# Kernel tuning notes

Hardware: AMD Instinct MI355X
Metric: run time of the kernel (lower is better)

The kernel has to match this reference:

```python
import jax, jax.numpy as jnp
import numpy as np

B, DE, T = 32, 256, 32
H, W, C = 128, 128, 128  # units == C


def setup_inputs() -> dict:
    key = jax.random.key(0)
    k1, k2, k3 = jax.random.split(key, 3)
    e = jax.random.normal(k1, (B, DE, T), dtype=jnp.float32)
    h = jax.random.normal(k2, (B, H, W, C), dtype=jnp.float32)
    Wd = jax.random.normal(k3, (DE, C), dtype=jnp.float32) * (1.0 / np.sqrt(DE))
    b = jnp.zeros((C,), dtype=jnp.float32)
    return {"e": e, "h": h, "Wd": Wd, "b": b}


def reference(e, h, Wd, b):
    # e: [B, DE, T]  -> dense over DE -> e_: [B, C, T]
    e_ = jnp.einsum('bdt,dc->bct', e, Wd) + b[None, :, None]
    Bh, Hh, Wh, Ch = h.shape
    HW = Hh * Wh
    # h NHWC -> [B, C, HW]
    h1 = h.transpose(0, 3, 1, 2).reshape(Bh, Ch, HW)
    # scores: [B, T, HW], contraction over channels
    s = jnp.einsum('bct,bcn->btn', e_, h1)
    # softmax over T (axis=1)
    beta = jax.nn.softmax(s, axis=1)
    # context: [B, C, HW]
    c = jnp.einsum('bct,btn->bcn', e_, beta)
    # -> [B, HW, C] -> NHWC
    c = c.transpose(0, 2, 1).reshape(Bh, Hh, Wh, Ch)
    return jnp.concatenate([c, h], axis=3)  # [B, H, W, 2C]
```

## Files before the change

### kernel.cpp

```cpp
#include <hip/hip_runtime.h>

typedef float v2f __attribute__((ext_vector_type(2)));

#define B_   32
#define DE_  256
#define T_   32
#define C_   128
#define HW_  16384

__device__ inline v2f vfma2(v2f a, v2f b, v2f c) {
#if __has_builtin(__builtin_elementwise_fma)
    return __builtin_elementwise_fma(a, b, c);
#else
    v2f r; r.x = fmaf(a.x, b.x, c.x); r.y = fmaf(a.y, b.y, c.y); return r;
#endif
}

__global__ __launch_bounds__(256) void dense_e_kernel(
    const float* __restrict__ e, const float* __restrict__ Wd,
    const float* __restrict__ bias, float* __restrict__ ews)
{
    __shared__ float elds[DE_ * T_];
    __shared__ float wlds[DE_ * 16];
    const int b   = blockIdx.y;
    const int cq  = blockIdx.x;
    const int tid = threadIdx.x;

    {
        const float4* erow = (const float4*)(e + ((size_t)b * DE_ + tid) * T_);
        float4* edst = (float4*)(elds + tid * T_);
        #pragma unroll
        for (int i = 0; i < 8; ++i) edst[i] = erow[i];

        const float4* wrow = (const float4*)(Wd + (size_t)tid * C_ + cq * 16);
        float4* wdst = (float4*)(wlds + tid * 16);
        #pragma unroll
        for (int i = 0; i < 4; ++i) wdst[i] = wrow[i];
    }
    __syncthreads();

    const int t  = tid & 31;
    const int c8 = tid >> 5;
    float a0 = 0.f, a1 = 0.f;
    #pragma unroll 8
    for (int d = 0; d < DE_; ++d) {
        float ev = elds[d * T_ + t];
        a0 = fmaf(ev, wlds[d * 16 + c8],     a0);
        a1 = fmaf(ev, wlds[d * 16 + 8 + c8], a1);
    }
    const int c0 = cq * 16 + c8;
    a0 += bias[c0];
    a1 += bias[c0 + 8];
    ews[((size_t)b * C_ + c0)     * T_ + t] = a0;
    ews[((size_t)b * C_ + c0 + 8) * T_ + t] = a1;
}

__global__ __launch_bounds__(256) void attn_fused_kernel(
    const float* __restrict__ h,
    const float* __restrict__ ews,
    float* __restrict__ out)
{
    const int b = blockIdx.x >> 6;
    const int n = ((blockIdx.x & 63) << 8) | threadIdx.x;
    const float* __restrict__ eb = ews + (size_t)b * (C_ * T_);
    const float4* hrow = (const float4*)(h + ((size_t)b * HW_ + n) * C_);
    float4* orow = (float4*)(out + ((size_t)b * HW_ + n) * (2 * C_));

    v2f s2[16];
    #pragma unroll
    for (int i = 0; i < 16; ++i) s2[i] = (v2f){0.f, 0.f};

    #pragma unroll 4
    for (int cb = 0; cb < 32; ++cb) {
        float4 hv = hrow[cb];
        orow[32 + cb] = hv;
        float hc[4] = {hv.x, hv.y, hv.z, hv.w};
        #pragma unroll
        for (int q = 0; q < 4; ++q) {
            const v2f* er = (const v2f*)(eb + (cb * 4 + q) * T_);
            v2f hb = {hc[q], hc[q]};
            #pragma unroll
            for (int tp = 0; tp < 16; ++tp) s2[tp] = vfma2(hb, er[tp], s2[tp]);
        }
    }

    v2f m2 = s2[0];
    #pragma unroll
    for (int i = 1; i < 16; ++i) {
        m2.x = fmaxf(m2.x, s2[i].x);
        m2.y = fmaxf(m2.y, s2[i].y);
    }
    const float m = fmaxf(m2.x, m2.y);
    float l = 0.f;
    #pragma unroll
    for (int i = 0; i < 16; ++i) {
        v2f p;
        p.x = __expf(s2[i].x - m);
        p.y = __expf(s2[i].y - m);
        s2[i] = p;
        l += p.x + p.y;
    }
    const float inv = 1.0f / l;
    #pragma unroll
    for (int i = 0; i < 16; ++i) { s2[i].x *= inv; s2[i].y *= inv; }

    #pragma unroll 4
    for (int cb = 0; cb < 32; ++cb) {
        float r[4];
        #pragma unroll
        for (int q = 0; q < 4; ++q) {
            const v2f* er = (const v2f*)(eb + (cb * 4 + q) * T_);
            v2f a = {0.f, 0.f};
            #pragma unroll
            for (int tp = 0; tp < 16; ++tp) a = vfma2(er[tp], s2[tp], a);
            r[q] = a.x + a.y;
        }
        float4 st = {r[0], r[1], r[2], r[3]};
        orow[cb] = st;
    }
}

extern "C" void kernel_launch(void* const* d_in, const int* in_sizes, int n_in,
                              void* d_out, int out_size, void* d_ws, size_t ws_size,
                              hipStream_t stream) {
    const float* e    = (const float*)d_in[0];
    const float* h    = (const float*)d_in[1];
    const float* Wd   = (const float*)d_in[2];
    const float* bias = (const float*)d_in[3];
    float* ews = (float*)d_ws;
    float* out = (float*)d_out;

    dense_e_kernel<<<dim3(8, 32), 256, 0, stream>>>(e, Wd, bias, ews);
    attn_fused_kernel<<<dim3(32 * (HW_ / 256)), 256, 0, stream>>>(h, ews, out);
}
```

Before: 910.4 us.

## Stage h loads and context stores through padded LDS for coalesced global access

The attention kernel previously had each thread read and write its own 512-byte pixel row, so a wavefront's global accesses were strided across rows. It now loads 32-channel slabs of h cooperatively with coalesced float4 reads and transposes them through padded shared memory. The context output goes back the same way before coalesced stores. This costs about 32KB of LDS per block, extra barriers and LDS traffic, which may lower occupancy.

```diff
diff --git a/kernel.cpp b/kernel.cpp
--- a/kernel.cpp
+++ b/kernel.cpp
@@ -7,6 +7,8 @@
 #define T_   32
 #define C_   128
 #define HW_  16384
+
+#define LSTRIDE 257
 
 __device__ inline v2f vfma2(v2f a, v2f b, v2f c) {
 #if __has_builtin(__builtin_elementwise_fma)
@@ -60,28 +62,48 @@
     const float* __restrict__ ews,
     float* __restrict__ out)
 {
-    const int b = blockIdx.x >> 6;
-    const int n = ((blockIdx.x & 63) << 8) | threadIdx.x;
+    __shared__ float lds[32 * LSTRIDE];
+    const int b   = blockIdx.x >> 6;
+    const int n0  = (blockIdx.x & 63) << 8;
+    const int tid = threadIdx.x;
     const float* __restrict__ eb = ews + (size_t)b * (C_ * T_);
-    const float4* hrow = (const float4*)(h + ((size_t)b * HW_ + n) * C_);
-    float4* orow = (float4*)(out + ((size_t)b * HW_ + n) * (2 * C_));
+    const float* __restrict__ hb = h   + ((size_t)b * HW_ + n0) * C_;
+    float* __restrict__       ob = out + ((size_t)b * HW_ + n0) * (2 * C_);
 
     v2f s2[16];
     #pragma unroll
     for (int i = 0; i < 16; ++i) s2[i] = (v2f){0.f, 0.f};
 
-    #pragma unroll 4
-    for (int cb = 0; cb < 32; ++cb) {
-        float4 hv = hrow[cb];
-        orow[32 + cb] = hv;
-        float hc[4] = {hv.x, hv.y, hv.z, hv.w};
+    for (int cb = 0; cb < 4; ++cb) {
+        float4 hv[8];
         #pragma unroll
-        for (int q = 0; q < 4; ++q) {
-            const v2f* er = (const v2f*)(eb + (cb * 4 + q) * T_);
-            v2f hb = {hc[q], hc[q]};
+        for (int i = 0; i < 8; ++i) {
+            const int idx = i * 256 + tid;
+            hv[i] = *(const float4*)(hb + (size_t)(idx >> 3) * C_ + cb * 32 + (idx & 7) * 4);
+        }
+        #pragma unroll
+        for (int i = 0; i < 8; ++i) {
+            const int idx = i * 256 + tid;
+            const int row = idx >> 3, c4 = idx & 7;
+            *(float4*)(ob + (size_t)row * (2 * C_) + C_ + cb * 32 + c4 * 4) = hv[i];
+            float* dst = lds + (c4 * 4) * LSTRIDE + row;
+            dst[0]           = hv[i].x;
+            dst[LSTRIDE]     = hv[i].y;
+            dst[2 * LSTRIDE] = hv[i].z;
+            dst[3 * LSTRIDE] = hv[i].w;
+        }
+        __syncthreads();
+
+        const float* ec = eb + (cb * 32) * T_;
+        #pragma unroll
+        for (int c = 0; c < 32; ++c) {
+            const float hc = lds[c * LSTRIDE + tid];
+            const v2f* er = (const v2f*)(ec + c * T_);
+            const v2f hbv = {hc, hc};
             #pragma unroll
-            for (int tp = 0; tp < 16; ++tp) s2[tp] = vfma2(hb, er[tp], s2[tp]);
+            for (int tp = 0; tp < 16; ++tp) s2[tp] = vfma2(hbv, er[tp], s2[tp]);
         }
+        __syncthreads();
     }
 
     v2f m2 = s2[0];
@@ -104,19 +126,25 @@
     #pragma unroll
     for (int i = 0; i < 16; ++i) { s2[i].x *= inv; s2[i].y *= inv; }
 
-    #pragma unroll 4
-    for (int cb = 0; cb < 32; ++cb) {
-        float r[4];
+    for (int cb = 0; cb < 4; ++cb) {
         #pragma unroll
-        for (int q = 0; q < 4; ++q) {
-            const v2f* er = (const v2f*)(eb + (cb * 4 + q) * T_);
+        for (int c = 0; c < 32; ++c) {
+            const v2f* er = (const v2f*)(eb + (size_t)(cb * 32 + c) * T_);
             v2f a = {0.f, 0.f};
             #pragma unroll
             for (int tp = 0; tp < 16; ++tp) a = vfma2(er[tp], s2[tp], a);
-            r[q] = a.x + a.y;
+            lds[c * LSTRIDE + tid] = a.x + a.y;
         }
-        float4 st = {r[0], r[1], r[2], r[3]};
-        orow[cb] = st;
+        __syncthreads();
+        #pragma unroll
+        for (int i = 0; i < 8; ++i) {
+            const int idx = i * 256 + tid;
+            const int row = idx >> 3, c4 = idx & 7;
+            const float* src = lds + (c4 * 4) * LSTRIDE + row;
+            float4 st = { src[0], src[LSTRIDE], src[2 * LSTRIDE], src[3 * LSTRIDE] };
+            *(float4*)(ob + (size_t)row * (2 * C_) + cb * 32 + c4 * 4) = st;
+        }
+        __syncthreads();
     }
 }
 
```

Result: no change. 905.0 us (-0.6%).
